# Kernel tuning notes

Hardware: AMD Instinct MI355X
Metric: run time of the kernel (lower is better)

Reference implementation:

```python
import jax, jax.numpy as jnp
import numpy as np

NUM_GROUPS = 32
EPS = 1e-5


def group_norm(x, gamma, beta):
    # x: (b, c, h, w)
    b, c, h, w = x.shape
    xg = x.reshape(b, NUM_GROUPS, c // NUM_GROUPS, h, w)
    mean = xg.mean(axis=(2, 3, 4), keepdims=True)
    var = xg.var(axis=(2, 3, 4), keepdims=True)
    xn = ((xg - mean) * jax.lax.rsqrt(var + EPS)).reshape(b, c, h, w)
    return xn * gamma[None, :, None, None] + beta[None, :, None, None]


def conv1x1(x, w, b):
    # 1x1 conv == channel matmul: x (b,c,h,w), w (out,in), b (out,)
    return jnp.einsum('bchw,oc->bohw', x, w) + b[None, :, None, None]


def setup_inputs() -> dict:
    key = jax.random.key(0)
    ks = jax.random.split(key, 10)
    C = 512
    x = jax.random.normal(ks[0], (16, C, 32, 32), dtype=jnp.float32)
    s = 1.0 / np.sqrt(C)
    return {
        'x': x,
        'norm_w': jnp.ones((C,), jnp.float32),
        'norm_b': jnp.zeros((C,), jnp.float32),
        'q_w': jax.random.normal(ks[1], (C, C), jnp.float32) * s,
        'q_b': jax.random.normal(ks[2], (C,), jnp.float32) * 0.01,
        'k_w': jax.random.normal(ks[3], (C, C), jnp.float32) * s,
        'k_b': jax.random.normal(ks[4], (C,), jnp.float32) * 0.01,
        'v_w': jax.random.normal(ks[5], (C, C), jnp.float32) * s,
        'v_b': jax.random.normal(ks[6], (C,), jnp.float32) * 0.01,
        'proj_w': jax.random.normal(ks[7], (C, C), jnp.float32) * s,
        'proj_b': jax.random.normal(ks[8], (C,), jnp.float32) * 0.01,
    }


def reference(x, norm_w, norm_b, q_w, q_b, k_w, k_b, v_w, v_b, proj_w, proj_b):
    b, c, h, w = x.shape
    hn = group_norm(x, norm_w, norm_b)
    q = conv1x1(hn, q_w, q_b).reshape(b, c, h * w)  # (b, c, n)
    k = conv1x1(hn, k_w, k_b).reshape(b, c, h * w)
    v = conv1x1(hn, v_w, v_b).reshape(b, c, h * w)
    scale = jnp.float32(c) ** -0.5
    # scores[b, i, j] = sum_c q[b,c,i] * k[b,c,j]
    scores = jnp.einsum('bci,bcj->bij', q, k) * scale  # (b, n, n)
    attn = jax.nn.softmax(scores, axis=-1)
    # h_[b, c, i] = sum_j v[b,c,j] * attn[b,i,j]
    out = jnp.einsum('bcj,bij->bci', v, attn).reshape(b, c, h, w)
    return x + conv1x1(out, proj_w, proj_b)
```

## Files before the change

### kernel.cpp

```cpp
#include <hip/hip_runtime.h>

#define B_ 16
#define C_ 512
#define N_ 1024

typedef __attribute__((ext_vector_type(8))) short bf16x8_t;
typedef __attribute__((ext_vector_type(4))) float f32x4_t;

__device__ __forceinline__ unsigned short f2bf(float f) {
  unsigned int u = __float_as_uint(f);
  u += 0x7fffu + ((u >> 16) & 1u);
  return (unsigned short)(u >> 16);
}

__device__ __forceinline__ f32x4_t mfma16(bf16x8_t a, bf16x8_t b, f32x4_t c) {
  return __builtin_amdgcn_mfma_f32_16x16x32_bf16(a, b, c, 0, 0, 0);
}

__device__ __forceinline__ void gload_lds16(const void* g, void* l) {
  __builtin_amdgcn_global_load_lds(
      (const __attribute__((address_space(1))) unsigned int*)g,
      (__attribute__((address_space(3))) unsigned int*)l, 16, 0, 0);
}

__global__ __launch_bounds__(256) void castw_k(
    const float* __restrict__ qw, const float* __restrict__ kw,
    const float* __restrict__ vw, const float* __restrict__ pw,
    unsigned short* __restrict__ Wqkv, unsigned short* __restrict__ Wp) {
  int i = (blockIdx.x * 256 + threadIdx.x) * 4;
  float4 a = *(const float4*)(qw + i);
  float4 b = *(const float4*)(kw + i);
  float4 c = *(const float4*)(vw + i);
  float4 d = *(const float4*)(pw + i);
  *(ushort4*)(Wqkv + i) = make_ushort4(f2bf(a.x), f2bf(a.y), f2bf(a.z), f2bf(a.w));
  *(ushort4*)(Wqkv + 262144 + i) =
      make_ushort4(f2bf(b.x), f2bf(b.y), f2bf(b.z), f2bf(b.w));
  *(ushort4*)(Wqkv + 524288 + i) =
      make_ushort4(f2bf(c.x), f2bf(c.y), f2bf(c.z), f2bf(c.w));
  *(ushort4*)(Wp + i) = make_ushort4(f2bf(d.x), f2bf(d.y), f2bf(d.z), f2bf(d.w));
}

__global__ __launch_bounds__(512, 1) void gn_fused_k(
    const float* __restrict__ x, const float* __restrict__ gw,
    const float* __restrict__ gb, unsigned short* __restrict__ hn) {
  int blk = blockIdx.x;
  int b = blk >> 4, gp = blk & 15;
  int t = threadIdx.x, lane = t & 63, wave = t >> 6;
  __shared__ float xs[32768];
  __shared__ float red[2][2][8];
  const float* xg = x + ((long)b * C_ + gp * 32) * N_;
  float s0 = 0.f, s20 = 0.f, s1 = 0.f, s21 = 0.f;
#pragma unroll
  for (int i = 0; i < 16; ++i) {
    int f4 = t + 512 * i;
    float4 v = ((const float4*)xg)[f4];
    float sum = v.x + v.y + v.z + v.w;
    float sq = v.x * v.x + v.y * v.y + v.z * v.z + v.w * v.w;
    if (i < 8) { s0 += sum; s20 += sq; } else { s1 += sum; s21 += sq; }
    int fi = f4 << 2;
    int c = fi >> 10, n = fi & 1023;
    int nx = n ^ (((c >> 3) & 3) << 4);
    *(float4*)&xs[(c << 10) + nx] = v;
  }
#pragma unroll
  for (int m = 1; m < 64; m <<= 1) {
    s0 += __shfl_xor(s0, m); s20 += __shfl_xor(s20, m);
    s1 += __shfl_xor(s1, m); s21 += __shfl_xor(s21, m);
  }
  if (lane == 0) {
    red[0][0][wave] = s0; red[1][0][wave] = s20;
    red[0][1][wave] = s1; red[1][1][wave] = s21;
  }
  __syncthreads();
  float m0 = 0.f, v0 = 0.f, m1 = 0.f, v1 = 0.f;
#pragma unroll
  for (int w = 0; w < 8; ++w) {
    m0 += red[0][0][w]; v0 += red[1][0][w];
    m1 += red[0][1][w]; v1 += red[1][1][w];
  }
  m0 *= (1.f / 16384.f); m1 *= (1.f / 16384.f);
  float rv0 = rsqrtf(v0 * (1.f / 16384.f) - m0 * m0 + 1e-5f);
  float rv1 = rsqrtf(v1 * (1.f / 16384.f) - m1 * m1 + 1e-5f);
  int q = t & 3;
  float mean = (q >> 1) ? m1 : m0, rv = (q >> 1) ? rv1 : rv0;
  float ga[8], be[8];
#pragma unroll
  for (int jj = 0; jj < 8; ++jj) {
    int gc = gp * 32 + q * 8 + jj;
    ga[jj] = gw[gc] * rv;
    be[jj] = gb[gc] - mean * ga[jj];
  }
  unsigned short* ob = hn + (long)b * N_ * C_ + gp * 32 + q * 8;
  int n0 = t >> 2;
  for (int it = 0; it < 8; ++it) {
    int n = n0 + (it << 7);
    int nsw = n ^ (q << 4);
    unsigned short us[8];
#pragma unroll
    for (int jj = 0; jj < 8; ++jj) {
      int c = q * 8 + jj;
      us[jj] = f2bf(xs[(c << 10) + nsw] * ga[jj] + be[jj]);
    }
    *(uint4*)(ob + (long)n * C_) = *(uint4*)us;
  }
}

__global__ __launch_bounds__(256) void gemm_qkv(
    const unsigned short* __restrict__ W, const unsigned short* __restrict__ HN,
    const float* __restrict__ qb, const float* __restrict__ kb,
    const float* __restrict__ vb, unsigned short* __restrict__ Q2,
    unsigned short* __restrict__ K2, unsigned short* __restrict__ V2,
    float scale) {
  int flat = blockIdx.x + 12 * (blockIdx.y + 8 * blockIdx.z);
  int nf = (flat & 7) * 192 + (flat >> 3);
  int bxi = nf % 12, rem = nf / 12;
  int byi = rem & 7, bz = rem >> 3;
  const unsigned short* Ab = W + (long)bxi * 128 * 512;
  const unsigned short* Bb = HN + (long)bz * N_ * C_ + (long)byi * 128 * 512;
  __shared__ char lds[32768];
  char* As = lds;
  char* Bs = lds + 16384;
  int tid = threadIdx.x;
  int lane = tid & 63, wave = tid >> 6;
  int wr = wave >> 1, wc = wave & 1;
  int lrow = lane & 15, kgrp = lane >> 4;
  int slab = bxi >> 2;
  f32x4_t acc[4][4];
#pragma unroll
  for (int i = 0; i < 4; ++i)
#pragma unroll
    for (int j = 0; j < 4; ++j) acc[i][j] = (f32x4_t){0.f, 0.f, 0.f, 0.f};

  int perm = (((lane & 7) ^ (lane >> 3)) << 3);
  const unsigned short* Asrc = Ab + (long)(wave * 32 + (lane >> 3)) * 512 + perm;
  const unsigned short* Bsrc = Bb + (long)(wave * 32 + (lane >> 3)) * 512 + perm;
  char* Adst = As + wave * 32 * 128;
  char* Bdst = Bs + wave * 32 * 128;

#pragma unroll
  for (int kt = 0; kt < 8; ++kt) {
    __syncthreads();
#pragma unroll
    for (int i = 0; i < 4; ++i) {
      gload_lds16(Asrc + (long)i * 8 * 512 + kt * 64, Adst + i * 1024);
      gload_lds16(Bsrc + (long)i * 8 * 512 + kt * 64, Bdst + i * 1024);
    }
    __syncthreads();
#pragma unroll
    for (int ks = 0; ks < 2; ++ks) {
      bf16x8_t af[4], bfv[4];
#pragma unroll
      for (int mi = 0; mi < 4; ++mi) {
        int r = wr * 64 + mi * 16 + lrow;
        int o = r * 128 + ks * 64 + kgrp * 16;
        o ^= (r & 7) << 4;
        af[mi] = *(bf16x8_t*)(As + o);
      }
#pragma unroll
      for (int ni = 0; ni < 4; ++ni) {
        int r = wc * 64 + ni * 16 + lrow;
        int o = r * 128 + ks * 64 + kgrp * 16;
        o ^= (r & 7) << 4;
        bfv[ni] = *(bf16x8_t*)(Bs + o);
      }
      if (slab < 2) {
#pragma unroll
        for (int mi = 0; mi < 4; ++mi)
#pragma unroll
          for (int ni = 0; ni < 4; ++ni)
            acc[mi][ni] = mfma16(af[mi], bfv[ni], acc[mi][ni]);
      } else {
#pragma unroll
        for (int ni = 0; ni < 4; ++ni)
#pragma unroll
          for (int mi = 0; mi < 4; ++mi)
            acc[ni][mi] = mfma16(bfv[ni], af[mi], acc[ni][mi]);
      }
    }
  }

  if (slab < 2) {
    const float* bias = slab == 0 ? qb : kb;
    float scl = slab == 0 ? scale : 1.f;
    int rowloc = (bxi & 3) * 128 + wr * 64;
    int colbase = byi * 128 + wc * 64;
    unsigned short* ob = (slab == 0 ? Q2 : K2) + ((long)bz << 19);
#pragma unroll
    for (int mi = 0; mi < 4; ++mi) {
#pragma unroll
      for (int ni = 0; ni < 4; ++ni) {
        int row0 = rowloc + mi * 16 + kgrp * 4;
        int col = colbase + ni * 16 + lrow;
        unsigned short us[4];
#pragma unroll
        for (int rg = 0; rg < 4; ++rg)
          us[rg] = f2bf((acc[mi][ni][rg] + bias[row0 + rg]) * scl);
        long off = ((long)(col >> 4) << 13) + ((long)(row0 >> 3) << 7) +
                   ((col & 15) << 3) + (row0 & 7);
        *(ushort4*)(ob + off) = make_ushort4(us[0], us[1], us[2], us[3]);
      }
    }
  } else {
    int cbase = (bxi & 3) * 128 + wr * 64;
    int nbase = byi * 128 + wc * 64;
    unsigned short* ob = V2 + ((long)bz << 19);
#pragma unroll
    for (int ni = 0; ni < 4; ++ni) {
#pragma unroll
      for (int mi = 0; mi < 4; ++mi) {
        int n0 = nbase + ni * 16 + kgrp * 4;
        int c = cbase + mi * 16 + lrow;
        float bv = vb[c];
        unsigned short us[4];
#pragma unroll
        for (int rg = 0; rg < 4; ++rg) us[rg] = f2bf(acc[ni][mi][rg] + bv);
        long off = ((long)(c >> 4) << 14) + ((long)(n0 >> 3) << 7) +
                   ((c & 15) << 3) + (n0 & 7);
        *(ushort4*)(ob + off) = make_ushort4(us[0], us[1], us[2], us[3]);
      }
    }
  }
}

__global__ __launch_bounds__(512, 1) void attn_pv_k(
    const unsigned short* __restrict__ q2, const unsigned short* __restrict__ k2,
    const unsigned short* __restrict__ v2, unsigned short* __restrict__ ao) {
  int f = blockIdx.x;
  int b = f & 15, ib = f >> 4;
  int tid = threadIdx.x, lane = tid & 63, wave = tid >> 6;
  int lrow = lane & 15, kgrp = lane >> 4;
  __shared__ unsigned short P2[65536];
  __shared__ float red1[8][64];
  __shared__ float invr[64];
  {
    const unsigned short* qsrc =
        q2 + ((long)b << 19) + ((long)(ib * 4) << 13) + wave * 4096 + lane * 8;
    char* qdst = (char*)P2 + wave * 8192;
#pragma unroll
    for (int i = 0; i < 8; ++i) gload_lds16(qsrc + i * 512, qdst + i * 1024);
  }
  asm volatile("s_waitcnt vmcnt(0)" ::: "memory");
  __syncthreads();
  f32x4_t acc[4][8];
#pragma unroll
  for (int h = 0; h < 4; ++h)
#pragma unroll
    for (int t = 0; t < 8; ++t) acc[h][t] = (f32x4_t){0.f, 0.f, 0.f, 0.f};
  const unsigned short* kb =
      k2 + ((long)b << 19) + ((long)(wave * 8) << 13) + lane * 8;
  for (int ks = 0; ks < 16; ++ks) {
    bf16x8_t kf[8];
#pragma unroll
    for (int t = 0; t < 8; ++t)
      kf[t] = *(const bf16x8_t*)(kb + t * 8192 + ks * 512);
    bf16x8_t qa[4];
#pragma unroll
    for (int h = 0; h < 4; ++h)
      qa[h] = *(const bf16x8_t*)&P2[h * 8192 + ks * 512 + lane * 8];
    __builtin_amdgcn_s_setprio(1);
#pragma unroll
    for (int h = 0; h < 4; ++h)
#pragma unroll
      for (int t = 0; t < 8; ++t) acc[h][t] = mfma16(kf[t], qa[h], acc[h][t]);
    __builtin_amdgcn_s_setprio(0);
  }
  __syncthreads();
  float sm[4] = {0.f, 0.f, 0.f, 0.f};
#pragma unroll
  for (int h = 0; h < 4; ++h) {
#pragma unroll
    for (int t = 0; t < 8; ++t) {
      int jb = wave * 16 + t * 2 + (kgrp >> 1);
      int off = h * 16384 + jb * 128 + (((lrow ^ (jb & 7)) << 3) | ((kgrp & 1) << 2));
      unsigned short us[4];
#pragma unroll
      for (int rg = 0; rg < 4; ++rg) {
        float p = exp2f(acc[h][t][rg]);
        sm[h] += p;
        us[rg] = f2bf(p);
      }
      *(ushort4*)&P2[off] = make_ushort4(us[0], us[1], us[2], us[3]);
    }
  }
#pragma unroll
  for (int m = 16; m < 64; m <<= 1)
#pragma unroll
    for (int h = 0; h < 4; ++h) sm[h] += __shfl_xor(sm[h], m);
  if (kgrp == 0) {
#pragma unroll
    for (int h = 0; h < 4; ++h) red1[wave][h * 16 + lrow] = sm[h];
  }
  __syncthreads();
  if (tid < 64) {
    float s = red1[0][tid];
#pragma unroll
    for (int w = 1; w < 8; ++w) s += red1[w][tid];
    invr[tid] = 1.f / s;
  }
  __syncthreads();
  f32x4_t o[4][4];
#pragma unroll
  for (int h = 0; h < 4; ++h)
#pragma unroll
    for (int cf = 0; cf < 4; ++cf) o[h][cf] = (f32x4_t){0.f, 0.f, 0.f, 0.f};
  const char* vb2 =
      (const char*)(v2 + ((long)b << 19) + ((long)(wave * 4) << 14)) + lane * 16;
  bf16x8_t vc[4];
#pragma unroll
  for (int cf = 0; cf < 4; ++cf) vc[cf] = *(const bf16x8_t*)(vb2 + cf * 32768);
#pragma unroll
  for (int js = 0; js < 32; ++js) {
    bf16x8_t vn[4];
    if (js < 31) {
#pragma unroll
      for (int cf = 0; cf < 4; ++cf)
        vn[cf] = *(const bf16x8_t*)(vb2 + cf * 32768 + (js + 1) * 1024);
    }
    int jb = js * 4 + kgrp;
    int pox = ((lrow ^ (jb & 7)) << 3) + jb * 128;
    bf16x8_t pa[4];
#pragma unroll
    for (int h = 0; h < 4; ++h)
      pa[h] = *(const bf16x8_t*)&P2[h * 16384 + pox];
    __builtin_amdgcn_s_setprio(1);
#pragma unroll
    for (int h = 0; h < 4; ++h)
#pragma unroll
      for (int cf = 0; cf < 4; ++cf)
        o[h][cf] = mfma16(pa[h], vc[cf], o[h][cf]);
    __builtin_amdgcn_s_setprio(0);
    if (js < 31) {
#pragma unroll
      for (int cf = 0; cf < 4; ++cf) vc[cf] = vn[cf];
    }
  }
  float inv[4][4];
#pragma unroll
  for (int h = 0; h < 4; ++h)
#pragma unroll
    for (int rg = 0; rg < 4; ++rg)
      inv[h][rg] = invr[h * 16 + kgrp * 4 + rg];
  unsigned short* aob = ao + ((long)(b * N_ + ib * 64)) * C_;
#pragma unroll
  for (int h = 0; h < 4; ++h)
#pragma unroll
    for (int cf = 0; cf < 4; ++cf) {
      int c = wave * 64 + cf * 16 + lrow;
#pragma unroll
      for (int rg = 0; rg < 4; ++rg) {
        int i = h * 16 + kgrp * 4 + rg;
        aob[(long)i * C_ + c] = f2bf(o[h][cf][rg] * inv[h][rg]);
      }
    }
}

__global__ __launch_bounds__(256) void gemm_proj(
    const unsigned short* __restrict__ A, const unsigned short* __restrict__ Bm,
    const float* __restrict__ bias, const float* __restrict__ resid,
    float* __restrict__ outp) {
  int flat = blockIdx.x + 4 * (blockIdx.y + 8 * blockIdx.z);
  int nf = (flat & 7) * 64 + (flat >> 3);
  int bxi = nf & 3, byi = (nf >> 2) & 7, bz = nf >> 5;
  const unsigned short* Ab = A + (long)bxi * 128 * 512;
  const unsigned short* Bb = Bm + (long)bz * N_ * C_ + (long)byi * 128 * 512;
  __shared__ char lds[32768];
  char* As = lds;
  char* Bs = lds + 16384;
  int tid = threadIdx.x;
  int lane = tid & 63, wave = tid >> 6;
  int wr = wave >> 1, wc = wave & 1;
  int lrow = lane & 15, kgrp = lane >> 4;
  f32x4_t acc[4][4];
#pragma unroll
  for (int i = 0; i < 4; ++i)
#pragma unroll
    for (int j = 0; j < 4; ++j) acc[i][j] = (f32x4_t){0.f, 0.f, 0.f, 0.f};

  int perm = (((lane & 7) ^ (lane >> 3)) << 3);
  const unsigned short* Asrc = Ab + (long)(wave * 32 + (lane >> 3)) * 512 + perm;
  const unsigned short* Bsrc = Bb + (long)(wave * 32 + (lane >> 3)) * 512 + perm;
  char* Adst = As + wave * 32 * 128;
  char* Bdst = Bs + wave * 32 * 128;

#pragma unroll
  for (int kt = 0; kt < 8; ++kt) {
    __syncthreads();
#pragma unroll
    for (int i = 0; i < 4; ++i) {
      gload_lds16(Asrc + (long)i * 8 * 512 + kt * 64, Adst + i * 1024);
      gload_lds16(Bsrc + (long)i * 8 * 512 + kt * 64, Bdst + i * 1024);
    }
    __syncthreads();
#pragma unroll
    for (int ks = 0; ks < 2; ++ks) {
      bf16x8_t af[4], bfv[4];
#pragma unroll
      for (int mi = 0; mi < 4; ++mi) {
        int r = wr * 64 + mi * 16 + lrow;
        int o = r * 128 + ks * 64 + kgrp * 16;
        o ^= (r & 7) << 4;
        af[mi] = *(bf16x8_t*)(As + o);
      }
#pragma unroll
      for (int ni = 0; ni < 4; ++ni) {
        int r = wc * 64 + ni * 16 + lrow;
        int o = r * 128 + ks * 64 + kgrp * 16;
        o ^= (r & 7) << 4;
        bfv[ni] = *(bf16x8_t*)(Bs + o);
      }
#pragma unroll
      for (int mi = 0; mi < 4; ++mi)
#pragma unroll
        for (int ni = 0; ni < 4; ++ni)
          acc[mi][ni] = mfma16(af[mi], bfv[ni], acc[mi][ni]);
    }
  }

  int rowbase = bxi * 128 + wr * 64;
  int colbase = byi * 128 + wc * 64;
  float* ob = outp + (long)bz * C_ * N_;
  const float* rb = resid + (long)bz * C_ * N_;
#pragma unroll
  for (int mi = 0; mi < 4; ++mi) {
#pragma unroll
    for (int ni = 0; ni < 4; ++ni) {
      int row0 = rowbase + mi * 16 + kgrp * 4;
      int col = colbase + ni * 16 + lrow;
#pragma unroll
      for (int rg = 0; rg < 4; ++rg) {
        int r = row0 + rg;
        ob[(long)r * N_ + col] =
            acc[mi][ni][rg] + bias[r] + rb[(long)r * N_ + col];
      }
    }
  }
}

extern "C" void kernel_launch(void* const* d_in, const int* in_sizes, int n_in,
                              void* d_out, int out_size, void* d_ws,
                              size_t ws_size, hipStream_t stream) {
  (void)in_sizes; (void)n_in; (void)out_size; (void)ws_size;
  const float* x = (const float*)d_in[0];
  const float* nw = (const float*)d_in[1];
  const float* nb = (const float*)d_in[2];
  const float* qw = (const float*)d_in[3];
  const float* qbias = (const float*)d_in[4];
  const float* kw = (const float*)d_in[5];
  const float* kbias = (const float*)d_in[6];
  const float* vw = (const float*)d_in[7];
  const float* vbias = (const float*)d_in[8];
  const float* pw = (const float*)d_in[9];
  const float* pbias = (const float*)d_in[10];
  float* out = (float*)d_out;

  char* ws = (char*)d_ws;
  unsigned short* WQKV = (unsigned short*)(ws + 0);
  unsigned short* Wp = (unsigned short*)(ws + 1572864);
  unsigned short* HN = (unsigned short*)(ws + 2097152);
  unsigned short* Q2 = (unsigned short*)(ws + 18874368);
  unsigned short* K2 = (unsigned short*)(ws + 35651584);
  unsigned short* V2 = (unsigned short*)(ws + 52428800);
  unsigned short* AO = (unsigned short*)(ws + 69206016);

  castw_k<<<256, 256, 0, stream>>>(qw, kw, vw, pw, WQKV, Wp);
  gn_fused_k<<<256, 512, 0, stream>>>(x, nw, nb, HN);

  const float scale = 0.06375871512f;
  gemm_qkv<<<dim3(12, 8, B_), 256, 0, stream>>>(WQKV, HN, qbias, kbias, vbias,
                                                Q2, K2, V2, scale);
  attn_pv_k<<<256, 512, 0, stream>>>(Q2, K2, V2, AO);
  gemm_proj<<<dim3(4, 8, B_), 256, 0, stream>>>(Wp, AO, pbias, x, out);
}
```

Measured before the change: 110.5 us.

## Pre-swizzle QKV weights into MFMA fragment layout and double-buffer HN tiles

Measured after the change: 128.2 us. 1.16x slower.

```diff
diff --git a/kernel.cpp b/kernel.cpp
--- a/kernel.cpp
+++ b/kernel.cpp
@@ -26,18 +26,27 @@
 __global__ __launch_bounds__(256) void castw_k(
     const float* __restrict__ qw, const float* __restrict__ kw,
     const float* __restrict__ vw, const float* __restrict__ pw,
-    unsigned short* __restrict__ Wqkv, unsigned short* __restrict__ Wp) {
-  int i = (blockIdx.x * 256 + threadIdx.x) * 4;
-  float4 a = *(const float4*)(qw + i);
-  float4 b = *(const float4*)(kw + i);
-  float4 c = *(const float4*)(vw + i);
-  float4 d = *(const float4*)(pw + i);
-  *(ushort4*)(Wqkv + i) = make_ushort4(f2bf(a.x), f2bf(a.y), f2bf(a.z), f2bf(a.w));
-  *(ushort4*)(Wqkv + 262144 + i) =
-      make_ushort4(f2bf(b.x), f2bf(b.y), f2bf(b.z), f2bf(b.w));
-  *(ushort4*)(Wqkv + 524288 + i) =
-      make_ushort4(f2bf(c.x), f2bf(c.y), f2bf(c.z), f2bf(c.w));
-  *(ushort4*)(Wp + i) = make_ushort4(f2bf(d.x), f2bf(d.y), f2bf(d.z), f2bf(d.w));
+    unsigned short* __restrict__ Wf, unsigned short* __restrict__ Wp) {
+  int idx = blockIdx.x * 256 + threadIdx.x;
+  int m = idx >> 6;
+  int k0 = (idx & 63) * 8;
+  long lin = (long)m * 512 + k0;
+  long foff = ((long)((m & 127) >> 4) << 13) + ((k0 >> 3) << 7) + ((m & 15) << 3);
+  int mt = m >> 7;
+#pragma unroll
+  for (int s = 0; s < 3; ++s) {
+    const float* src = s == 0 ? qw : (s == 1 ? kw : vw);
+    float4 a = *(const float4*)(src + lin);
+    float4 b2 = *(const float4*)(src + lin + 4);
+    unsigned short us[8] = {f2bf(a.x),  f2bf(a.y),  f2bf(a.z),  f2bf(a.w),
+                            f2bf(b2.x), f2bf(b2.y), f2bf(b2.z), f2bf(b2.w)};
+    *(uint4*)(Wf + (long)(s * 4 + mt) * 65536 + foff) = *(uint4*)us;
+  }
+  float4 d = *(const float4*)(pw + lin);
+  float4 d2 = *(const float4*)(pw + lin + 4);
+  unsigned short up[8] = {f2bf(d.x),  f2bf(d.y),  f2bf(d.z),  f2bf(d.w),
+                          f2bf(d2.x), f2bf(d2.y), f2bf(d2.z), f2bf(d2.w)};
+  *(uint4*)(Wp + lin) = *(uint4*)up;
 }
 
 __global__ __launch_bounds__(512, 1) void gn_fused_k(
@@ -106,7 +115,7 @@
 }
 
 __global__ __launch_bounds__(256) void gemm_qkv(
-    const unsigned short* __restrict__ W, const unsigned short* __restrict__ HN,
+    const unsigned short* __restrict__ Wf, const unsigned short* __restrict__ HN,
     const float* __restrict__ qb, const float* __restrict__ kb,
     const float* __restrict__ vb, unsigned short* __restrict__ Q2,
     unsigned short* __restrict__ K2, unsigned short* __restrict__ V2,
@@ -115,11 +124,8 @@
   int nf = (flat & 7) * 192 + (flat >> 3);
   int bxi = nf % 12, rem = nf / 12;
   int byi = rem & 7, bz = rem >> 3;
-  const unsigned short* Ab = W + (long)bxi * 128 * 512;
   const unsigned short* Bb = HN + (long)bz * N_ * C_ + (long)byi * 128 * 512;
   __shared__ char lds[32768];
-  char* As = lds;
-  char* Bs = lds + 16384;
   int tid = threadIdx.x;
   int lane = tid & 63, wave = tid >> 6;
   int wr = wave >> 1, wc = wave & 1;
@@ -131,52 +137,77 @@
 #pragma unroll
     for (int j = 0; j < 4; ++j) acc[i][j] = (f32x4_t){0.f, 0.f, 0.f, 0.f};
 
+  const unsigned short* Af =
+      Wf + (long)bxi * 65536 + (long)(wr * 4) * 8192 + lane * 8;
+
   int perm = (((lane & 7) ^ (lane >> 3)) << 3);
-  const unsigned short* Asrc = Ab + (long)(wave * 32 + (lane >> 3)) * 512 + perm;
   const unsigned short* Bsrc = Bb + (long)(wave * 32 + (lane >> 3)) * 512 + perm;
-  char* Adst = As + wave * 32 * 128;
-  char* Bdst = Bs + wave * 32 * 128;
-
-#pragma unroll
+  char* Bdst0 = lds + wave * 4096;
+  char* Bdst1 = lds + 16384 + wave * 4096;
+
+#pragma unroll
+  for (int i = 0; i < 4; ++i)
+    gload_lds16(Bsrc + (long)i * 8 * 512, Bdst0 + i * 1024);
+  __syncthreads();
+
   for (int kt = 0; kt < 8; ++kt) {
+    char* cur = lds + ((kt & 1) ? 16384 : 0);
+    char* nxtd = ((kt & 1) ? Bdst0 : Bdst1);
+    bf16x8_t af0[4];
+#pragma unroll
+    for (int mi = 0; mi < 4; ++mi)
+      af0[mi] = *(const bf16x8_t*)(Af + mi * 8192 + (kt * 2) * 512);
+    if (kt < 7) {
+#pragma unroll
+      for (int i = 0; i < 4; ++i)
+        gload_lds16(Bsrc + (long)i * 8 * 512 + (kt + 1) * 64, nxtd + i * 1024);
+    }
+    bf16x8_t bfv[4];
+#pragma unroll
+    for (int ni = 0; ni < 4; ++ni) {
+      int r = wc * 64 + ni * 16 + lrow;
+      int o = r * 128 + kgrp * 16;
+      o ^= (r & 7) << 4;
+      bfv[ni] = *(bf16x8_t*)(cur + o);
+    }
+    if (slab < 2) {
+#pragma unroll
+      for (int mi = 0; mi < 4; ++mi)
+#pragma unroll
+        for (int ni = 0; ni < 4; ++ni)
+          acc[mi][ni] = mfma16(af0[mi], bfv[ni], acc[mi][ni]);
+    } else {
+#pragma unroll
+      for (int ni = 0; ni < 4; ++ni)
+#pragma unroll
+        for (int mi = 0; mi < 4; ++mi)
+          acc[ni][mi] = mfma16(bfv[ni], af0[mi], acc[ni][mi]);
+    }
+    bf16x8_t af1[4];
+#pragma unroll
+    for (int mi = 0; mi < 4; ++mi)
+      af1[mi] = *(const bf16x8_t*)(Af + mi * 8192 + (kt * 2 + 1) * 512);
+#pragma unroll
+    for (int ni = 0; ni < 4; ++ni) {
+      int r = wc * 64 + ni * 16 + lrow;
+      int o = r * 128 + 64 + kgrp * 16;
+      o ^= (r & 7) << 4;
+      bfv[ni] = *(bf16x8_t*)(cur + o);
+    }
+    if (slab < 2) {
+#pragma unroll
+      for (int mi = 0; mi < 4; ++mi)
+#pragma unroll
+        for (int ni = 0; ni < 4; ++ni)
+          acc[mi][ni] = mfma16(af1[mi], bfv[ni], acc[mi][ni]);
+    } else {
+#pragma unroll
+      for (int ni = 0; ni < 4; ++ni)
+#pragma unroll
+        for (int mi = 0; mi < 4; ++mi)
+          acc[ni][mi] = mfma16(bfv[ni], af1[mi], acc[ni][mi]);
+    }
     __syncthreads();
-#pragma unroll
-    for (int i = 0; i < 4; ++i) {
-      gload_lds16(Asrc + (long)i * 8 * 512 + kt * 64, Adst + i * 1024);
-      gload_lds16(Bsrc + (long)i * 8 * 512 + kt * 64, Bdst + i * 1024);
-    }
-    __syncthreads();
-#pragma unroll
-    for (int ks = 0; ks < 2; ++ks) {
-      bf16x8_t af[4], bfv[4];
-#pragma unroll
-      for (int mi = 0; mi < 4; ++mi) {
-        int r = wr * 64 + mi * 16 + lrow;
-        int o = r * 128 + ks * 64 + kgrp * 16;
-        o ^= (r & 7) << 4;
-        af[mi] = *(bf16x8_t*)(As + o);
-      }
-#pragma unroll
-      for (int ni = 0; ni < 4; ++ni) {
-        int r = wc * 64 + ni * 16 + lrow;
-        int o = r * 128 + ks * 64 + kgrp * 16;
-        o ^= (r & 7) << 4;
-        bfv[ni] = *(bf16x8_t*)(Bs + o);
-      }
-      if (slab < 2) {
-#pragma unroll
-        for (int mi = 0; mi < 4; ++mi)
-#pragma unroll
-          for (int ni = 0; ni < 4; ++ni)
-            acc[mi][ni] = mfma16(af[mi], bfv[ni], acc[mi][ni]);
-      } else {
-#pragma unroll
-        for (int ni = 0; ni < 4; ++ni)
-#pragma unroll
-          for (int mi = 0; mi < 4; ++mi)
-            acc[ni][mi] = mfma16(bfv[ni], af[mi], acc[ni][mi]);
-      }
-    }
   }
 
   if (slab < 2) {
@@ -382,7 +413,6 @@
   char* Adst = As + wave * 32 * 128;
   char* Bdst = Bs + wave * 32 * 128;
 
-#pragma unroll
   for (int kt = 0; kt < 8; ++kt) {
     __syncthreads();
 #pragma unroll
@@ -454,7 +484,7 @@
   float* out = (float*)d_out;
 
   char* ws = (char*)d_ws;
-  unsigned short* WQKV = (unsigned short*)(ws + 0);
+  unsigned short* WQKVf = (unsigned short*)(ws + 0);
   unsigned short* Wp = (unsigned short*)(ws + 1572864);
   unsigned short* HN = (unsigned short*)(ws + 2097152);
   unsigned short* Q2 = (unsigned short*)(ws + 18874368);
@@ -462,11 +492,11 @@
   unsigned short* V2 = (unsigned short*)(ws + 52428800);
   unsigned short* AO = (unsigned short*)(ws + 69206016);
 
-  castw_k<<<256, 256, 0, stream>>>(qw, kw, vw, pw, WQKV, Wp);
+  castw_k<<<128, 256, 0, stream>>>(qw, kw, vw, pw, WQKVf, Wp);
   gn_fused_k<<<256, 512, 0, stream>>>(x, nw, nb, HN);
 
   const float scale = 0.06375871512f;
-  gemm_qkv<<<dim3(12, 8, B_), 256, 0, stream>>>(WQKV, HN, qbias, kbias, vbias,
+  gemm_qkv<<<dim3(12, 8, B_), 256, 0, stream>>>(WQKVf, HN, qbias, kbias, vbias,
                                                 Q2, K2, V2, scale);
   attn_pv_k<<<256, 512, 0, stream>>>(Q2, K2, V2, AO);
   gemm_proj<<<dim3(4, 8, B_), 256, 0, stream>>>(Wp, AO, pbias, x, out);
```
